# Kernel tuning notes

Hardware: AMD Instinct MI355X
Metric: run time of the kernel (lower is better)

## Reference

```python
import jax, jax.numpy as jnp
import numpy as np

N_NODES = 50000
N_EDGES = 600000
IN_DIM = 4
HID = 128
N_LAYERS = 6
BN_EPS = 1e-5


def setup_inputs() -> dict:
    key = jax.random.key(0)
    ks = jax.random.split(key, 20)
    x = jax.random.normal(ks[0], (N_NODES, IN_DIM), dtype=jnp.float32)
    edge_index = jax.random.randint(ks[1], (2, N_EDGES), 0, N_NODES, dtype=jnp.int32)
    s = 0.05
    return {
        "x": x,
        "edge_index": edge_index,
        "enc_w": jax.random.normal(ks[2], (IN_DIM, HID), jnp.float32) * s,
        "enc_b": jnp.zeros((HID,), jnp.float32),
        "enc_bn_g": jnp.ones((HID,), jnp.float32),
        "enc_bn_b": jnp.zeros((HID,), jnp.float32),
        "conv_w": jax.random.normal(ks[3], (N_LAYERS, HID, HID), jnp.float32) * s,
        "conv_b": jnp.zeros((N_LAYERS, HID), jnp.float32),
        "bn_g": jnp.ones((N_LAYERS, HID), jnp.float32),
        "bn_b": jnp.zeros((N_LAYERS, HID), jnp.float32),
        "dec_w1": jax.random.normal(ks[4], (HID, HID // 2), jnp.float32) * s,
        "dec_b1": jnp.zeros((HID // 2,), jnp.float32),
        "dec_w2": jax.random.normal(ks[5], (HID // 2, HID // 4), jnp.float32) * s,
        "dec_b2": jnp.zeros((HID // 4,), jnp.float32),
        "dec_w3": jax.random.normal(ks[6], (HID // 4, 1), jnp.float32) * s,
        "dec_b3": jnp.zeros((1,), jnp.float32),
    }


def _batchnorm(h, g, b):
    # training-mode BatchNorm1d over node axis (biased variance, like torch)
    mu = h.mean(axis=0)
    var = jnp.mean(jnp.square(h - mu), axis=0)
    return (h - mu) * jax.lax.rsqrt(var + BN_EPS) * g + b


def _gcn_conv(h, W, b, src, dst, inv_sqrt_deg, n):
    # PyG GCNConv: sym-normalized A+I aggregation, aggregate at dst
    hw = h @ W                                   # [N, HID]
    norm = inv_sqrt_deg[src] * inv_sqrt_deg[dst]  # [E]
    msg = hw[src] * norm[:, None]                # [E, HID] (dominant traffic)
    agg = jax.ops.segment_sum(msg, dst, num_segments=n)
    self_loop = hw * jnp.square(inv_sqrt_deg)[:, None]
    return agg + self_loop + b


def reference(x, edge_index, enc_w, enc_b, enc_bn_g, enc_bn_b,
              conv_w, conv_b, bn_g, bn_b,
              dec_w1, dec_b1, dec_w2, dec_b2, dec_w3, dec_b3):
    n = x.shape[0]
    src, dst = edge_index[0], edge_index[1]
    # degree includes self loop (A + I)
    deg = jax.ops.segment_sum(jnp.ones_like(dst, dtype=x.dtype), dst, num_segments=n) + 1.0
    inv_sqrt_deg = jax.lax.rsqrt(deg)

    # encoder: Linear -> ReLU -> BatchNorm (dropout = identity in eval)
    h = jax.nn.relu(x @ enc_w + enc_b)
    h = _batchnorm(h, enc_bn_g, enc_bn_b)

    for l in range(N_LAYERS):
        h_new = _gcn_conv(h, conv_w[l], conv_b[l], src, dst, inv_sqrt_deg, n)
        h_new = jax.nn.relu(_batchnorm(h_new, bn_g[l], bn_b[l]))
        h = h + h_new  # residual

    # decoder MLP
    d = jax.nn.relu(h @ dec_w1 + dec_b1)
    d = jax.nn.relu(d @ dec_w2 + dec_b2)
    out = d @ dec_w3 + dec_b3
    return out.squeeze(-1)  # [N]
```

## Files before the change

kernel.cpp:

```cpp
#include <hip/hip_runtime.h>

#define BN_EPS 1e-5f

typedef unsigned int uint_t;
typedef unsigned short ushort_t;
typedef short bf16x8 __attribute__((ext_vector_type(8)));
typedef float f32x4 __attribute__((ext_vector_type(4)));

__device__ __forceinline__ float bflo(uint_t v) { return __uint_as_float(v << 16); }
__device__ __forceinline__ float bfhi(uint_t v) { return __uint_as_float(v & 0xffff0000u); }
__device__ __forceinline__ uint_t f2bf(float f) {
    uint_t u = __float_as_uint(f);
    u += 0x7fffu + ((u >> 16) & 1u);
    return u >> 16;
}

__device__ __forceinline__ void acc8(float* a, uint4 g, float w) {
    a[0] = fmaf(bflo(g.x), w, a[0]);
    a[1] = fmaf(bfhi(g.x), w, a[1]);
    a[2] = fmaf(bflo(g.y), w, a[2]);
    a[3] = fmaf(bfhi(g.y), w, a[3]);
    a[4] = fmaf(bflo(g.z), w, a[4]);
    a[5] = fmaf(bfhi(g.z), w, a[5]);
    a[6] = fmaf(bflo(g.w), w, a[6]);
    a[7] = fmaf(bfhi(g.w), w, a[7]);
}


__global__ void count_kernel(const int* __restrict__ ei, int* __restrict__ counts, int E) {
    int e = blockIdx.x * blockDim.x + threadIdx.x;
    if (e < E) atomicAdd(&counts[ei[E + e]], 1);
}

__global__ __launch_bounds__(256) void scan_part(const int* __restrict__ counts,
                                                 int* __restrict__ rowptr, int* __restrict__ bsum,
                                                 float* __restrict__ isd, int n) {
    const int tid = threadIdx.x;
    const int lane = tid & 63, wave = tid >> 6;
    __shared__ int wsum[4];
    int idx0 = blockIdx.x * 2048 + tid * 8;
    int v[8];
    int tsum = 0;
#pragma unroll
    for (int j = 0; j < 8; j++) {
        int i = idx0 + j;
        int c = (i < n) ? counts[i] : 0;
        if (i < n) isd[i] = rsqrtf((float)c + 1.0f);
        v[j] = (i < n) ? (((c + 4) >> 2) << 2) : 0;
        tsum += v[j];
    }
    int incl = tsum;
#pragma unroll
    for (int off = 1; off < 64; off <<= 1) {
        int t = __shfl_up(incl, off, 64);
        if (lane >= off) incl += t;
    }
    if (lane == 63) wsum[wave] = incl;
    __syncthreads();
    int wexcl = 0;
    for (int w2 = 0; w2 < wave; w2++) wexcl += wsum[w2];
    int run = wexcl + (incl - tsum);
#pragma unroll
    for (int j = 0; j < 8; j++) {
        int i = idx0 + j;
        if (i < n) rowptr[i] = run;
        run += v[j];
    }
    if (tid == 255) bsum[blockIdx.x] = run;
}

__global__ void scan_mid(int* __restrict__ bsum, int nb) {
    int lane = threadIdx.x;
    int v = (lane < nb) ? bsum[lane] : 0;
    int incl = v;
#pragma unroll
    for (int off = 1; off < 64; off <<= 1) {
        int t = __shfl_up(incl, off, 64);
        if (lane >= off) incl += t;
    }
    if (lane < nb) bsum[lane] = incl - v;
    if (lane == 63) bsum[nb] = incl;
}

__global__ void scan_add_self(int* __restrict__ rowptr, const int* __restrict__ bsum,
                              const int* __restrict__ counts, const float* __restrict__ isd,
                              int2* __restrict__ edges, int n, int nb) {
    int i = blockIdx.x * 256 + threadIdx.x;
    if (i < n) {
        int rp = rowptr[i] + bsum[i >> 11];
        rowptr[i] = rp;
        int c = counts[i];
        int pos = rp + c;
        int end = rp + (((c + 4) >> 2) << 2);
        float v = isd[i];
        edges[pos] = make_int2(i, __float_as_int(v * v));
        for (int p = pos + 1; p < end; p++) edges[p] = make_int2(i, 0);
    } else if (i == n) {
        rowptr[n] = bsum[nb];
    }
}

__global__ void scatter_kernel(const int* __restrict__ ei, const int* __restrict__ rowptr,
                               int* __restrict__ cursor, const float* __restrict__ isd,
                               int2* __restrict__ edges, int E) {
    int e = blockIdx.x * blockDim.x + threadIdx.x;
    if (e < E) {
        int s = ei[e], d = ei[E + e];
        int p = atomicAdd(&cursor[d], 1);
        edges[rowptr[d] + p] = make_int2(s, __float_as_int(isd[s] * isd[d]));
    }
}


__global__ void wtrans_kernel(const float* __restrict__ W, ushort_t* __restrict__ Wt) {
    int id = blockIdx.x * 256 + threadIdx.x;
    int l = id >> 14, rem = id & 16383;
    int k = rem >> 7, n = rem & 127;
    Wt[(l << 14) + (n << 7) + k] = f2bf(W[id]);
}


__global__ __launch_bounds__(256) void encoder_kernel(const float* __restrict__ x,
                                                      const float* __restrict__ W,
                                                      const float* __restrict__ b,
                                                      float* __restrict__ h0,
                                                      float* __restrict__ stats, int N) {
    int tid = threadIdx.x;
    int g = blockIdx.x * 256 + tid;
    int total = gridDim.x * 256;
    int c = tid & 127;
    float w0 = W[c], w1 = W[128 + c], w2 = W[256 + c], w3 = W[384 + c], bb = b[c];
    float s = 0.f, q = 0.f;
    int tot = N * 128;
    for (int i = g; i < tot; i += total) {
        int n = i >> 7;
        float4 xv = ((const float4*)x)[n];
        float v = fmaf(xv.x, w0, fmaf(xv.y, w1, fmaf(xv.z, w2, fmaf(xv.w, w3, bb))));
        v = fmaxf(v, 0.f);
        h0[i] = v;
        s += v;
        q += v * v;
    }
    __shared__ float ls[256];
    ls[tid] = s;
    __syncthreads();
    if (tid < 128) atomicAdd(&stats[tid], ls[tid] + ls[tid + 128]);
    __syncthreads();
    ls[tid] = q;
    __syncthreads();
    if (tid < 128) atomicAdd(&stats[128 + tid], ls[tid] + ls[tid + 128]);
}


#define SWZ(byte, row) ((byte) ^ (((row) & 7) << 4))

template <int MODE>
__global__ __launch_bounds__(512) void mfma_gemm(const float* __restrict__ h,
                                                 const ushort_t* __restrict__ aggb,
                                                 const float* __restrict__ stats,
                                                 const float* __restrict__ g,
                                                 const float* __restrict__ beta, float invN,
                                                 const ushort_t* __restrict__ Wt,
                                                 float* __restrict__ hout,
                                                 ushort_t* __restrict__ hwb, int N) {
    __shared__ ushort_t As[128 * 128];
    __shared__ float s_sc[128], s_sh[128];
    const int tid = threadIdx.x;
    const int row0 = blockIdx.x * 128;

    if (tid < 128) {
        float S = stats[tid], Q = stats[tid + 128];
        float mu = S * invN;
        float var = fmaxf(Q * invN - mu * mu, 0.f);
        float rs = rsqrtf(var + BN_EPS);
        float sc = g[tid] * rs;
        s_sc[tid] = sc;
        s_sh[tid] = beta[tid] - mu * sc;
    }
    __syncthreads();

#pragma unroll
    for (int j = 0; j < 4; j++) {
        int idx = (j * 512 + tid) * 8;
        int r = idx >> 7, c = idx & 127;
        int grow = row0 + r;
        float av[8] = {0.f, 0.f, 0.f, 0.f, 0.f, 0.f, 0.f, 0.f};
        if (grow < N) {
            float4 h0 = *(const float4*)&h[(size_t)grow * 128 + c];
            float4 h1 = *(const float4*)&h[(size_t)grow * 128 + c + 4];
            float hv[8] = {h0.x, h0.y, h0.z, h0.w, h1.x, h1.y, h1.z, h1.w};
            if (MODE == 0) {
#pragma unroll
                for (int k = 0; k < 8; k++) av[k] = fmaf(hv[k], s_sc[c + k], s_sh[c + k]);
            } else {
                uint4 ag = *(const uint4*)&aggb[(size_t)grow * 128 + c];
                float ga[8] = {bflo(ag.x), bfhi(ag.x), bflo(ag.y), bfhi(ag.y),
                               bflo(ag.z), bfhi(ag.z), bflo(ag.w), bfhi(ag.w)};
#pragma unroll
                for (int k = 0; k < 8; k++)
                    av[k] = hv[k] + fmaxf(fmaf(ga[k], s_sc[c + k], s_sh[c + k]), 0.f);
            }
            *(float4*)&hout[(size_t)grow * 128 + c] = make_float4(av[0], av[1], av[2], av[3]);
            *(float4*)&hout[(size_t)grow * 128 + c + 4] = make_float4(av[4], av[5], av[6], av[7]);
        }
        uint4 p;
        p.x = f2bf(av[0]) | (f2bf(av[1]) << 16);
        p.y = f2bf(av[2]) | (f2bf(av[3]) << 16);
        p.z = f2bf(av[4]) | (f2bf(av[5]) << 16);
        p.w = f2bf(av[6]) | (f2bf(av[7]) << 16);
        *(uint4*)((char*)As + SWZ(r * 256 + c * 2, r)) = p;
    }
    __syncthreads();

    const int w = tid >> 6, l = tid & 63;
    const int mrow = l & 15, kg = l >> 4;
    const int arow = w * 16 + mrow;
    bf16x8 afr[4];
#pragma unroll
    for (int ks = 0; ks < 4; ks++)
        afr[ks] = *(const bf16x8*)((const char*)As + SWZ(arow * 256 + ks * 64 + kg * 16, arow));

    f32x4 acc[8];
#pragma unroll
    for (int nt = 0; nt < 8; nt++) acc[nt] = (f32x4){0.f, 0.f, 0.f, 0.f};

#pragma unroll
    for (int nt = 0; nt < 8; nt++) {
        const ushort_t* wp = &Wt[(size_t)(nt * 16 + mrow) * 128 + kg * 8];
#pragma unroll
        for (int ks = 0; ks < 4; ks++) {
            bf16x8 bfr = *(const bf16x8*)&wp[ks * 32];
            acc[nt] = __builtin_amdgcn_mfma_f32_16x16x32_bf16(afr[ks], bfr, acc[nt], 0, 0, 0);
        }
    }

#pragma unroll
    for (int nt = 0; nt < 8; nt++) {
#pragma unroll
        for (int r = 0; r < 4; r++) {
            int grow = row0 + w * 16 + kg * 4 + r;
            if (grow < N) hwb[(size_t)grow * 128 + nt * 16 + mrow] = f2bf(acc[nt][r]);
        }
    }
}


template <int K, int NOUT, int MODE, bool RELU>
__global__ __launch_bounds__(256) void fused_gemm(const float* __restrict__ A0,
                                                  const ushort_t* __restrict__ aggb,
                                                  const float* __restrict__ stats,
                                                  const float* __restrict__ g,
                                                  const float* __restrict__ beta, float invN,
                                                  const float* __restrict__ B,
                                                  const float* __restrict__ bias,
                                                  float* __restrict__ Cf, int N) {
    constexpr int TN = NOUT / 16;
    constexpr int LDA = K + 1;
    __shared__ float As[64 * LDA];
    __shared__ float Bs[16 * NOUT];
    __shared__ float s_sc[128], s_sh[128];
    const int tid = threadIdx.x;
    const int row0 = blockIdx.x * 64;

    if (MODE == 1) {
        if (tid < 128) {
            float S = stats[tid], Q = stats[tid + 128];
            float mu = S * invN;
            float var = fmaxf(Q * invN - mu * mu, 0.f);
            float rs = rsqrtf(var + BN_EPS);
            float sc = g[tid] * rs;
            s_sc[tid] = sc;
            s_sh[tid] = beta[tid] - mu * sc;
        }
        __syncthreads();
#pragma unroll
        for (int j = 0; j < 4; j++) {
            int idx = (j * 256 + tid) * 8;
            int r = idx >> 7, c = idx & 127;
            int grow = row0 + r;
            float av[8] = {0.f, 0.f, 0.f, 0.f, 0.f, 0.f, 0.f, 0.f};
            if (grow < N) {
                float4 h0 = *(const float4*)&A0[(size_t)grow * 128 + c];
                float4 h1 = *(const float4*)&A0[(size_t)grow * 128 + c + 4];
                float hv[8] = {h0.x, h0.y, h0.z, h0.w, h1.x, h1.y, h1.z, h1.w};
                uint4 ag = *(const uint4*)&aggb[(size_t)grow * 128 + c];
                float ga[8] = {bflo(ag.x), bfhi(ag.x), bflo(ag.y), bfhi(ag.y),
                               bflo(ag.z), bfhi(ag.z), bflo(ag.w), bfhi(ag.w)};
#pragma unroll
                for (int k = 0; k < 8; k++)
                    av[k] = hv[k] + fmaxf(fmaf(ga[k], s_sc[c + k], s_sh[c + k]), 0.f);
            }
#pragma unroll
            for (int k = 0; k < 8; k++) As[r * LDA + c + k] = av[k];
        }
    } else {
        constexpr int NF4 = 64 * K / 4 / 256;
#pragma unroll
        for (int j = 0; j < NF4; j++) {
            int idx = (j * 256 + tid) * 4;
            int r = idx / K;
            int c = idx % K;
            int grow = row0 + r;
            float4 a = make_float4(0.f, 0.f, 0.f, 0.f);
            if (grow < N) a = *(const float4*)&A0[(size_t)grow * K + c];
            As[r * LDA + c + 0] = a.x;
            As[r * LDA + c + 1] = a.y;
            As[r * LDA + c + 2] = a.z;
            As[r * LDA + c + 3] = a.w;
        }
    }
    __syncthreads();

    float acc[4][TN];
#pragma unroll
    for (int i = 0; i < 4; i++)
#pragma unroll
        for (int j = 0; j < TN; j++) acc[i][j] = 0.f;

    const int tx = tid & 15, ty = tid >> 4;
    for (int k0 = 0; k0 < K; k0 += 16) {
        for (int f = tid; f < 16 * NOUT / 4; f += 256) {
            int r = f / (NOUT / 4), c4 = (f % (NOUT / 4)) * 4;
            *(float4*)&Bs[r * NOUT + c4] = *(const float4*)&B[(size_t)(k0 + r) * NOUT + c4];
        }
        __syncthreads();
#pragma unroll
        for (int kk = 0; kk < 16; ++kk) {
            float a[4], bf[TN];
#pragma unroll
            for (int i = 0; i < 4; i++) a[i] = As[(ty * 4 + i) * LDA + k0 + kk];
#pragma unroll
            for (int j = 0; j < TN; j++) bf[j] = Bs[kk * NOUT + tx * TN + j];
#pragma unroll
            for (int i = 0; i < 4; i++)
#pragma unroll
                for (int j = 0; j < TN; j++) acc[i][j] = fmaf(a[i], bf[j], acc[i][j]);
        }
        __syncthreads();
    }

#pragma unroll
    for (int i = 0; i < 4; i++) {
        int grow = row0 + ty * 4 + i;
        if (grow >= N) continue;
#pragma unroll
        for (int j = 0; j < TN; j++) {
            int c = tx * TN + j;
            float v = acc[i][j];
            if (bias) v += bias[c];
            if (RELU) v = fmaxf(v, 0.f);
            Cf[(size_t)grow * NOUT + c] = v;
        }
    }
}


__global__ __launch_bounds__(256) void agg_kernel(const ushort_t* __restrict__ hwb,
                                                  const int* __restrict__ rowptr,
                                                  const int2* __restrict__ edges,
                                                  ushort_t* __restrict__ aggb,
                                                  float* __restrict__ stats, int N) {
    const int tid = threadIdx.x;
    const int wave = tid >> 6, lane = tid & 63;
    const int cbase = (lane & 15) * 8;
    const int gid = blockIdx.x * 16 + (tid >> 4);
    const int G = gridDim.x * 16;
    float s[8], q[8];
#pragma unroll
    for (int j = 0; j < 8; j++) {
        s[j] = 0.f;
        q[j] = 0.f;
    }

    for (int n = gid; n < N; n += G) {
        const int e0 = rowptr[n], e1 = rowptr[n + 1];
        float a[8] = {0.f, 0.f, 0.f, 0.f, 0.f, 0.f, 0.f, 0.f};
        for (int e = e0; e < e1; e += 16) {
            int c0 = min(e, e1 - 4);
            int c1 = min(e + 4, e1 - 4);
            int c2 = min(e + 8, e1 - 4);
            int c3 = min(e + 12, e1 - 4);
            int4 p0a = *(const int4*)&edges[c0];
            int4 p0b = *(const int4*)&edges[c0 + 2];
            int4 p1a = *(const int4*)&edges[c1];
            int4 p1b = *(const int4*)&edges[c1 + 2];
            int4 p2a = *(const int4*)&edges[c2];
            int4 p2b = *(const int4*)&edges[c2 + 2];
            int4 p3a = *(const int4*)&edges[c3];
            int4 p3b = *(const int4*)&edges[c3 + 2];
            float4 wv0 = make_float4(__int_as_float(p0a.y), __int_as_float(p0a.w),
                                     __int_as_float(p0b.y), __int_as_float(p0b.w));
            float4 wv1 = make_float4(__int_as_float(p1a.y), __int_as_float(p1a.w),
                                     __int_as_float(p1b.y), __int_as_float(p1b.w));
            float4 wv2 = make_float4(__int_as_float(p2a.y), __int_as_float(p2a.w),
                                     __int_as_float(p2b.y), __int_as_float(p2b.w));
            float4 wv3 = make_float4(__int_as_float(p3a.y), __int_as_float(p3a.w),
                                     __int_as_float(p3b.y), __int_as_float(p3b.w));
            if (e + 4 >= e1) wv1 = make_float4(0.f, 0.f, 0.f, 0.f);
            if (e + 8 >= e1) wv2 = make_float4(0.f, 0.f, 0.f, 0.f);
            if (e + 12 >= e1) wv3 = make_float4(0.f, 0.f, 0.f, 0.f);
            uint4 g0 = *(const uint4*)&hwb[(size_t)p0a.x * 128 + cbase];
            uint4 g1 = *(const uint4*)&hwb[(size_t)p0a.z * 128 + cbase];
            uint4 g2 = *(const uint4*)&hwb[(size_t)p0b.x * 128 + cbase];
            uint4 g3 = *(const uint4*)&hwb[(size_t)p0b.z * 128 + cbase];
            uint4 g4 = *(const uint4*)&hwb[(size_t)p1a.x * 128 + cbase];
            uint4 g5 = *(const uint4*)&hwb[(size_t)p1a.z * 128 + cbase];
            uint4 g6 = *(const uint4*)&hwb[(size_t)p1b.x * 128 + cbase];
            uint4 g7 = *(const uint4*)&hwb[(size_t)p1b.z * 128 + cbase];
            uint4 g8 = *(const uint4*)&hwb[(size_t)p2a.x * 128 + cbase];
            uint4 g9 = *(const uint4*)&hwb[(size_t)p2a.z * 128 + cbase];
            uint4 g10 = *(const uint4*)&hwb[(size_t)p2b.x * 128 + cbase];
            uint4 g11 = *(const uint4*)&hwb[(size_t)p2b.z * 128 + cbase];
            uint4 g12 = *(const uint4*)&hwb[(size_t)p3a.x * 128 + cbase];
            uint4 g13 = *(const uint4*)&hwb[(size_t)p3a.z * 128 + cbase];
            uint4 g14 = *(const uint4*)&hwb[(size_t)p3b.x * 128 + cbase];
            uint4 g15 = *(const uint4*)&hwb[(size_t)p3b.z * 128 + cbase];
            acc8(a, g0, wv0.x);
            acc8(a, g1, wv0.y);
            acc8(a, g2, wv0.z);
            acc8(a, g3, wv0.w);
            acc8(a, g4, wv1.x);
            acc8(a, g5, wv1.y);
            acc8(a, g6, wv1.z);
            acc8(a, g7, wv1.w);
            acc8(a, g8, wv2.x);
            acc8(a, g9, wv2.y);
            acc8(a, g10, wv2.z);
            acc8(a, g11, wv2.w);
            acc8(a, g12, wv3.x);
            acc8(a, g13, wv3.y);
            acc8(a, g14, wv3.z);
            acc8(a, g15, wv3.w);
        }
        uint4 p;
        p.x = f2bf(a[0]) | (f2bf(a[1]) << 16);
        p.y = f2bf(a[2]) | (f2bf(a[3]) << 16);
        p.z = f2bf(a[4]) | (f2bf(a[5]) << 16);
        p.w = f2bf(a[6]) | (f2bf(a[7]) << 16);
        *(uint4*)&aggb[(size_t)n * 128 + cbase] = p;
#pragma unroll
        for (int j = 0; j < 8; j++) {
            s[j] += a[j];
            q[j] += a[j] * a[j];
        }
    }

#pragma unroll
    for (int j = 0; j < 8; j++) {
        s[j] += __shfl_xor(s[j], 16, 64);
        s[j] += __shfl_xor(s[j], 32, 64);
        q[j] += __shfl_xor(q[j], 16, 64);
        q[j] += __shfl_xor(q[j], 32, 64);
    }
    __shared__ float ls[4][128];
    if (lane < 16) {
#pragma unroll
        for (int j = 0; j < 8; j++) ls[wave][cbase + j] = s[j];
    }
    __syncthreads();
    if (tid < 128) atomicAdd(&stats[tid], ls[0][tid] + ls[1][tid] + ls[2][tid] + ls[3][tid]);
    __syncthreads();
    if (lane < 16) {
#pragma unroll
        for (int j = 0; j < 8; j++) ls[wave][cbase + j] = q[j];
    }
    __syncthreads();
    if (tid < 128) atomicAdd(&stats[128 + tid], ls[0][tid] + ls[1][tid] + ls[2][tid] + ls[3][tid]);
}


__global__ void dec3_kernel(const float* __restrict__ d2, const float* __restrict__ W3,
                            const float* __restrict__ b3, float* __restrict__ out, int N) {
    __shared__ float tile[64 * 33];
    __shared__ float w3s[32];
    int base = blockIdx.x * 64;
    int tid = threadIdx.x;
    if (tid < 32) w3s[tid] = W3[tid];
    for (int f = tid; f < 2048; f += 256) {
        int r = f >> 5, c = f & 31;
        int n = base + r;
        tile[r * 33 + c] = (n < N) ? d2[(size_t)n * 32 + c] : 0.f;
    }
    __syncthreads();
    if (tid < 64) {
        int n = base + tid;
        if (n < N) {
            float s = b3[0];
#pragma unroll
            for (int k = 0; k < 32; k++) s = fmaf(tile[tid * 33 + k], w3s[k], s);
            out[n] = s;
        }
    }
}


extern "C" void kernel_launch(void* const* d_in, const int* in_sizes, int n_in, void* d_out,
                              int out_size, void* d_ws, size_t ws_size, hipStream_t stream) {
    const float* x = (const float*)d_in[0];
    const int* ei = (const int*)d_in[1];
    const float* enc_w = (const float*)d_in[2];
    const float* enc_b = (const float*)d_in[3];
    const float* enc_bn_g = (const float*)d_in[4];
    const float* enc_bn_b = (const float*)d_in[5];
    const float* conv_w = (const float*)d_in[6];
    const float* bn_g = (const float*)d_in[8];
    const float* bn_b = (const float*)d_in[9];
    const float* dw1 = (const float*)d_in[10];
    const float* db1 = (const float*)d_in[11];
    const float* dw2 = (const float*)d_in[12];
    const float* db2 = (const float*)d_in[13];
    const float* dw3 = (const float*)d_in[14];
    const float* db3 = (const float*)d_in[15];
    float* out = (float*)d_out;

    const int N = in_sizes[0] / 4;
    const int E = in_sizes[1] / 2;
    const size_t N128 = (size_t)N * 128;
    const int EPMAX = E + 4 * N;
    const float invN = 1.0f / N;

    float* h = (float*)d_ws;
    ushort_t* aggb = (ushort_t*)(h + N128);
    ushort_t* hwb = aggb + N128;
    ushort_t* wt = hwb + N128;
    float* stats = (float*)(wt + 6 * 16384);
    float* isd = stats + 7 * 256;
    int* counts = (int*)(isd + N);
    int* rowptr = counts + N;
    int* cursor = rowptr + N + 1;
    int* bsum = cursor + N;
    int2* edges = (int2*)(bsum + 66);
    float* d1 = (float*)hwb;
    float* d2 = (float*)aggb;

    (void)hipMemsetAsync(stats, 0, 7 * 256 * sizeof(float), stream);
    (void)hipMemsetAsync(counts, 0, (size_t)N * sizeof(int), stream);
    (void)hipMemsetAsync(cursor, 0, (size_t)N * sizeof(int), stream);

    const int eb = (E + 255) / 256;
    const int snb = (N + 2047) / 2048;
    count_kernel<<<eb, 256, 0, stream>>>(ei, counts, E);
    scan_part<<<snb, 256, 0, stream>>>(counts, rowptr, bsum, isd, N);
    scan_mid<<<1, 64, 0, stream>>>(bsum, snb);
    scan_add_self<<<(N + 256) / 256, 256, 0, stream>>>(rowptr, bsum, counts, isd, edges, N, snb);
    scatter_kernel<<<eb, 256, 0, stream>>>(ei, rowptr, cursor, isd, edges, E);
    wtrans_kernel<<<384, 256, 0, stream>>>(conv_w, wt);

    encoder_kernel<<<1024, 256, 0, stream>>>(x, enc_w, enc_b, h, stats, N);

    const int mblocks = (N + 127) / 128;
    const int gblocks = (N + 63) / 64;
    const int ablocks = 512;

    mfma_gemm<0><<<mblocks, 512, 0, stream>>>(h, nullptr, stats, enc_bn_g, enc_bn_b, invN, wt, h,
                                              hwb, N);
    agg_kernel<<<ablocks, 256, 0, stream>>>(hwb, rowptr, edges, aggb, stats + 256, N);

    for (int l = 1; l < 6; l++) {
        mfma_gemm<1><<<mblocks, 512, 0, stream>>>(h, aggb, stats + l * 256, bn_g + (l - 1) * 128,
                                                  bn_b + (l - 1) * 128, invN,
                                                  wt + (size_t)l * 16384, h, hwb, N);
        agg_kernel<<<ablocks, 256, 0, stream>>>(hwb, rowptr, edges, aggb, stats + (l + 1) * 256,
                                                N);
    }

    fused_gemm<128, 64, 1, true><<<gblocks, 256, 0, stream>>>(
        h, aggb, stats + 6 * 256, bn_g + 5 * 128, bn_b + 5 * 128, invN, dw1, db1, d1, N);
    fused_gemm<64, 32, 2, true><<<gblocks, 256, 0, stream>>>(d1, nullptr, nullptr, nullptr,
                                                             nullptr, 0.f, dw2, db2, d2, N);
    dec3_kernel<<<gblocks, 256, 0, stream>>>(d2, dw3, db3, out, N);
}
```

Measured before the change: 525.6 us.

## Fuse decoder layers 2-3, init scatter cursor from rowptr, raise agg grid

Fuses the second and third decoder layers into one kernel, so the 32-wide intermediate stays in shared memory instead of going through global memory and a separate launch. The scatter cursor is now initialised to rowptr in the scan kernel, which removes a memset and a rowptr load per edge. The aggregation grid grows from 512 to 768 blocks, and the edge buffer is aligned to 16 bytes. The risks are small: the fused kernel uses more shared memory, which may lower occupancy.

Result: no change. 531.3 us (+1.1%).

```diff
diff --git a/kernel.cpp b/kernel.cpp
--- a/kernel.cpp
+++ b/kernel.cpp
@@ -84,11 +84,12 @@
 
 __global__ void scan_add_self(int* __restrict__ rowptr, const int* __restrict__ bsum,
                               const int* __restrict__ counts, const float* __restrict__ isd,
-                              int2* __restrict__ edges, int n, int nb) {
+                              int* __restrict__ cursor, int2* __restrict__ edges, int n, int nb) {
     int i = blockIdx.x * 256 + threadIdx.x;
     if (i < n) {
         int rp = rowptr[i] + bsum[i >> 11];
         rowptr[i] = rp;
+        cursor[i] = rp;
         int c = counts[i];
         int pos = rp + c;
         int end = rp + (((c + 4) >> 2) << 2);
@@ -100,14 +101,13 @@
     }
 }
 
-__global__ void scatter_kernel(const int* __restrict__ ei, const int* __restrict__ rowptr,
-                               int* __restrict__ cursor, const float* __restrict__ isd,
-                               int2* __restrict__ edges, int E) {
+__global__ void scatter_kernel(const int* __restrict__ ei, int* __restrict__ cursor,
+                               const float* __restrict__ isd, int2* __restrict__ edges, int E) {
     int e = blockIdx.x * blockDim.x + threadIdx.x;
     if (e < E) {
         int s = ei[e], d = ei[E + e];
-        int p = atomicAdd(&cursor[d], 1);
-        edges[rowptr[d] + p] = make_int2(s, __float_as_int(isd[s] * isd[d]));
+        int idx = atomicAdd(&cursor[d], 1);
+        edges[idx] = make_int2(s, __float_as_int(isd[s] * isd[d]));
     }
 }
 
@@ -245,16 +245,15 @@
 }
 
 
-template <int K, int NOUT, int MODE, bool RELU>
-__global__ __launch_bounds__(256) void fused_gemm(const float* __restrict__ A0,
-                                                  const ushort_t* __restrict__ aggb,
-                                                  const float* __restrict__ stats,
-                                                  const float* __restrict__ g,
-                                                  const float* __restrict__ beta, float invN,
-                                                  const float* __restrict__ B,
-                                                  const float* __restrict__ bias,
-                                                  float* __restrict__ Cf, int N) {
-    constexpr int TN = NOUT / 16;
+__global__ __launch_bounds__(256) void dec1_kernel(const float* __restrict__ A0,
+                                                   const ushort_t* __restrict__ aggb,
+                                                   const float* __restrict__ stats,
+                                                   const float* __restrict__ g,
+                                                   const float* __restrict__ beta, float invN,
+                                                   const float* __restrict__ B,
+                                                   const float* __restrict__ bias,
+                                                   float* __restrict__ Cf, int N) {
+    constexpr int K = 128, NOUT = 64, TN = NOUT / 16;
     constexpr int LDA = K + 1;
     __shared__ float As[64 * LDA];
     __shared__ float Bs[16 * NOUT];
@@ -262,52 +261,35 @@
     const int tid = threadIdx.x;
     const int row0 = blockIdx.x * 64;
 
-    if (MODE == 1) {
-        if (tid < 128) {
-            float S = stats[tid], Q = stats[tid + 128];
-            float mu = S * invN;
-            float var = fmaxf(Q * invN - mu * mu, 0.f);
-            float rs = rsqrtf(var + BN_EPS);
-            float sc = g[tid] * rs;
-            s_sc[tid] = sc;
-            s_sh[tid] = beta[tid] - mu * sc;
-        }
-        __syncthreads();
-#pragma unroll
-        for (int j = 0; j < 4; j++) {
-            int idx = (j * 256 + tid) * 8;
-            int r = idx >> 7, c = idx & 127;
-            int grow = row0 + r;
-            float av[8] = {0.f, 0.f, 0.f, 0.f, 0.f, 0.f, 0.f, 0.f};
-            if (grow < N) {
-                float4 h0 = *(const float4*)&A0[(size_t)grow * 128 + c];
-                float4 h1 = *(const float4*)&A0[(size_t)grow * 128 + c + 4];
-                float hv[8] = {h0.x, h0.y, h0.z, h0.w, h1.x, h1.y, h1.z, h1.w};
-                uint4 ag = *(const uint4*)&aggb[(size_t)grow * 128 + c];
-                float ga[8] = {bflo(ag.x), bfhi(ag.x), bflo(ag.y), bfhi(ag.y),
-                               bflo(ag.z), bfhi(ag.z), bflo(ag.w), bfhi(ag.w)};
-#pragma unroll
-                for (int k = 0; k < 8; k++)
-                    av[k] = hv[k] + fmaxf(fmaf(ga[k], s_sc[c + k], s_sh[c + k]), 0.f);
-            }
-#pragma unroll
-            for (int k = 0; k < 8; k++) As[r * LDA + c + k] = av[k];
-        }
-    } else {
-        constexpr int NF4 = 64 * K / 4 / 256;
-#pragma unroll
-        for (int j = 0; j < NF4; j++) {
-            int idx = (j * 256 + tid) * 4;
-            int r = idx / K;
-            int c = idx % K;
-            int grow = row0 + r;
-            float4 a = make_float4(0.f, 0.f, 0.f, 0.f);
-            if (grow < N) a = *(const float4*)&A0[(size_t)grow * K + c];
-            As[r * LDA + c + 0] = a.x;
-            As[r * LDA + c + 1] = a.y;
-            As[r * LDA + c + 2] = a.z;
-            As[r * LDA + c + 3] = a.w;
-        }
+    if (tid < 128) {
+        float S = stats[tid], Q = stats[tid + 128];
+        float mu = S * invN;
+        float var = fmaxf(Q * invN - mu * mu, 0.f);
+        float rs = rsqrtf(var + BN_EPS);
+        float sc = g[tid] * rs;
+        s_sc[tid] = sc;
+        s_sh[tid] = beta[tid] - mu * sc;
+    }
+    __syncthreads();
+#pragma unroll
+    for (int j = 0; j < 4; j++) {
+        int idx = (j * 256 + tid) * 8;
+        int r = idx >> 7, c = idx & 127;
+        int grow = row0 + r;
+        float av[8] = {0.f, 0.f, 0.f, 0.f, 0.f, 0.f, 0.f, 0.f};
+        if (grow < N) {
+            float4 h0 = *(const float4*)&A0[(size_t)grow * 128 + c];
+            float4 h1 = *(const float4*)&A0[(size_t)grow * 128 + c + 4];
+            float hv[8] = {h0.x, h0.y, h0.z, h0.w, h1.x, h1.y, h1.z, h1.w};
+            uint4 ag = *(const uint4*)&aggb[(size_t)grow * 128 + c];
+            float ga[8] = {bflo(ag.x), bfhi(ag.x), bflo(ag.y), bfhi(ag.y),
+                           bflo(ag.z), bfhi(ag.z), bflo(ag.w), bfhi(ag.w)};
+#pragma unroll
+            for (int k = 0; k < 8; k++)
+                av[k] = hv[k] + fmaxf(fmaf(ga[k], s_sc[c + k], s_sh[c + k]), 0.f);
+        }
+#pragma unroll
+        for (int k = 0; k < 8; k++) As[r * LDA + c + k] = av[k];
     }
     __syncthreads();
 
@@ -346,10 +328,80 @@
 #pragma unroll
         for (int j = 0; j < TN; j++) {
             int c = tx * TN + j;
-            float v = acc[i][j];
-            if (bias) v += bias[c];
-            if (RELU) v = fmaxf(v, 0.f);
-            Cf[(size_t)grow * NOUT + c] = v;
+            Cf[(size_t)grow * NOUT + c] = fmaxf(acc[i][j] + bias[c], 0.f);
+        }
+    }
+}
+
+
+__global__ __launch_bounds__(256) void dec23_kernel(const float* __restrict__ d1,
+                                                    const float* __restrict__ dw2,
+                                                    const float* __restrict__ db2,
+                                                    const float* __restrict__ dw3,
+                                                    const float* __restrict__ db3,
+                                                    float* __restrict__ out, int N) {
+    constexpr int K = 64, NOUT = 32, TN = 2;
+    __shared__ float As[64 * (K + 1)];
+    __shared__ float Bs[K * NOUT];
+    __shared__ float t2[64 * 33];
+    __shared__ float w3s[32];
+    const int tid = threadIdx.x;
+    const int row0 = blockIdx.x * 64;
+
+    if (tid < 32) w3s[tid] = dw3[tid];
+#pragma unroll
+    for (int j = 0; j < 4; j++) {
+        int idx = (j * 256 + tid) * 4;
+        int r = idx >> 6, c = idx & 63;
+        int grow = row0 + r;
+        float4 a = make_float4(0.f, 0.f, 0.f, 0.f);
+        if (grow < N) a = *(const float4*)&d1[(size_t)grow * K + c];
+        As[r * (K + 1) + c + 0] = a.x;
+        As[r * (K + 1) + c + 1] = a.y;
+        As[r * (K + 1) + c + 2] = a.z;
+        As[r * (K + 1) + c + 3] = a.w;
+    }
+#pragma unroll
+    for (int j = 0; j < 2; j++) {
+        int f = (j * 256 + tid) * 4;
+        *(float4*)&Bs[f] = *(const float4*)&dw2[f];
+    }
+    __syncthreads();
+
+    const int tx = tid & 15, ty = tid >> 4;
+    float acc[4][TN];
+#pragma unroll
+    for (int i = 0; i < 4; i++)
+#pragma unroll
+        for (int j = 0; j < TN; j++) acc[i][j] = 0.f;
+#pragma unroll
+    for (int kk = 0; kk < K; ++kk) {
+        float a[4], bf[TN];
+#pragma unroll
+        for (int i = 0; i < 4; i++) a[i] = As[(ty * 4 + i) * (K + 1) + kk];
+#pragma unroll
+        for (int j = 0; j < TN; j++) bf[j] = Bs[kk * NOUT + tx * TN + j];
+#pragma unroll
+        for (int i = 0; i < 4; i++)
+#pragma unroll
+            for (int j = 0; j < TN; j++) acc[i][j] = fmaf(a[i], bf[j], acc[i][j]);
+    }
+#pragma unroll
+    for (int i = 0; i < 4; i++) {
+#pragma unroll
+        for (int j = 0; j < TN; j++) {
+            int c = tx * TN + j;
+            t2[(ty * 4 + i) * 33 + c] = fmaxf(acc[i][j] + db2[c], 0.f);
+        }
+    }
+    __syncthreads();
+    if (tid < 64) {
+        int n = row0 + tid;
+        if (n < N) {
+            float s = db3[0];
+#pragma unroll
+            for (int k = 0; k < 32; k++) s = fmaf(t2[tid * 33 + k], w3s[k], s);
+            out[n] = s;
         }
     }
 }
@@ -469,31 +521,6 @@
 }
 
 
-__global__ void dec3_kernel(const float* __restrict__ d2, const float* __restrict__ W3,
-                            const float* __restrict__ b3, float* __restrict__ out, int N) {
-    __shared__ float tile[64 * 33];
-    __shared__ float w3s[32];
-    int base = blockIdx.x * 64;
-    int tid = threadIdx.x;
-    if (tid < 32) w3s[tid] = W3[tid];
-    for (int f = tid; f < 2048; f += 256) {
-        int r = f >> 5, c = f & 31;
-        int n = base + r;
-        tile[r * 33 + c] = (n < N) ? d2[(size_t)n * 32 + c] : 0.f;
-    }
-    __syncthreads();
-    if (tid < 64) {
-        int n = base + tid;
-        if (n < N) {
-            float s = b3[0];
-#pragma unroll
-            for (int k = 0; k < 32; k++) s = fmaf(tile[tid * 33 + k], w3s[k], s);
-            out[n] = s;
-        }
-    }
-}
-
-
 extern "C" void kernel_launch(void* const* d_in, const int* in_sizes, int n_in, void* d_out,
                               int out_size, void* d_ws, size_t ws_size, hipStream_t stream) {
     const float* x = (const float*)d_in[0];
@@ -516,7 +543,6 @@
     const int N = in_sizes[0] / 4;
     const int E = in_sizes[1] / 2;
     const size_t N128 = (size_t)N * 128;
-    const int EPMAX = E + 4 * N;
     const float invN = 1.0f / N;
 
     float* h = (float*)d_ws;
@@ -529,28 +555,28 @@
     int* rowptr = counts + N;
     int* cursor = rowptr + N + 1;
     int* bsum = cursor + N;
-    int2* edges = (int2*)(bsum + 66);
+    int2* edges = (int2*)(((uintptr_t)(bsum + 66) + 15) & ~(uintptr_t)15);
     float* d1 = (float*)hwb;
     float* d2 = (float*)aggb;
 
     (void)hipMemsetAsync(stats, 0, 7 * 256 * sizeof(float), stream);
     (void)hipMemsetAsync(counts, 0, (size_t)N * sizeof(int), stream);
-    (void)hipMemsetAsync(cursor, 0, (size_t)N * sizeof(int), stream);
 
     const int eb = (E + 255) / 256;
     const int snb = (N + 2047) / 2048;
     count_kernel<<<eb, 256, 0, stream>>>(ei, counts, E);
     scan_part<<<snb, 256, 0, stream>>>(counts, rowptr, bsum, isd, N);
     scan_mid<<<1, 64, 0, stream>>>(bsum, snb);
-    scan_add_self<<<(N + 256) / 256, 256, 0, stream>>>(rowptr, bsum, counts, isd, edges, N, snb);
-    scatter_kernel<<<eb, 256, 0, stream>>>(ei, rowptr, cursor, isd, edges, E);
+    scan_add_self<<<(N + 256) / 256, 256, 0, stream>>>(rowptr, bsum, counts, isd, cursor, edges,
+                                                       N, snb);
+    scatter_kernel<<<eb, 256, 0, stream>>>(ei, cursor, isd, edges, E);
     wtrans_kernel<<<384, 256, 0, stream>>>(conv_w, wt);
 
     encoder_kernel<<<1024, 256, 0, stream>>>(x, enc_w, enc_b, h, stats, N);
 
     const int mblocks = (N + 127) / 128;
     const int gblocks = (N + 63) / 64;
-    const int ablocks = 512;
+    const int ablocks = 768;
 
     mfma_gemm<0><<<mblocks, 512, 0, stream>>>(h, nullptr, stats, enc_bn_g, enc_bn_b, invN, wt, h,
                                               hwb, N);
@@ -564,9 +590,8 @@
                                                 N);
     }
 
-    fused_gemm<128, 64, 1, true><<<gblocks, 256, 0, stream>>>(
-        h, aggb, stats + 6 * 256, bn_g + 5 * 128, bn_b + 5 * 128, invN, dw1, db1, d1, N);
-    fused_gemm<64, 32, 2, true><<<gblocks, 256, 0, stream>>>(d1, nullptr, nullptr, nullptr,
-                                                             nullptr, 0.f, dw2, db2, d2, N);
-    dec3_kernel<<<gblocks, 256, 0, stream>>>(d2, dw3, db3, out, N);
-}
+    dec1_kernel<<<gblocks, 256, 0, stream>>>(h, aggb, stats + 6 * 256, bn_g + 5 * 128,
+                                             bn_b + 5 * 128, invN, dw1, db1, d1, N);
+    dec23_kernel<<<gblocks, 256, 0, stream>>>(d1, dw2, db2, dw3, db3, out, N);
+    (void)d2;
+}
```
